# Kernel tuning notes

Hardware: AMD Instinct MI355X
Metric: run time of the kernel (lower is better)

The kernel has to match this reference:

```python
import jax, jax.numpy as jnp
import numpy as np

B, K, L, D = 64, 64, 128, 128  # batch, top_k, max_length, embedding_dimension
H = 2 * D                      # MLP input size (context || gathered entity)
N_HIDDEN = 6                   # Linear(H,H) layers with Tanh (dropout is eval no-op)


def setup_inputs() -> dict:
    key = jax.random.key(0)
    k0, k1, k2 = jax.random.split(key, 3)
    context = jax.random.normal(k0, (B, K, 2, L, D), dtype=jnp.float32)
    Ws = jax.random.normal(k1, (N_HIDDEN, H, H), dtype=jnp.float32) * 0.05
    bs = jnp.zeros((N_HIDDEN, H), dtype=jnp.float32)
    W_out = jax.random.normal(k2, (H,), dtype=jnp.float32) * 0.05
    b_out = jnp.zeros((), dtype=jnp.float32)
    return {"context": context, "Ws": Ws, "bs": bs, "W_out": W_out, "b_out": b_out}


def reference(context, Ws, bs, W_out, b_out):
    ctx = context[:, :, 0]  # [B,K,L,D]
    ent = context[:, :, 1]  # [B,K,L,D]
    cn = jnp.linalg.norm(ctx, axis=-1, keepdims=True)  # [B,K,L,1]
    en = jnp.linalg.norm(ent, axis=-1, keepdims=True)  # [B,K,L,1]
    # cosine-similarity matrix between context rows and entity rows
    sim = jnp.einsum("bkld,bkmd->bklm", ctx, ent) / (cn * jnp.swapaxes(en, -1, -2))
    ctx_n = ctx / cn
    ent_n = ent / en
    idx = jnp.argmax(sim, axis=-1)  # [B,K,L] top-1 entity row per context row
    gathered = jnp.take_along_axis(
        ent_n, jnp.broadcast_to(idx[..., None], ent_n.shape), axis=2
    )  # [B,K,L,D]
    # stack(...,-2) then flatten(start_dim=-2) == concat along feature dim
    x = jnp.concatenate([ctx_n, gathered], axis=-1)  # [B,K,L,2D]
    for i in range(N_HIDDEN):
        x = jnp.tanh(x @ Ws[i].T + bs[i])
    out = x @ W_out + b_out  # [B,K,L]
    return jnp.sum(out, axis=-1)  # [B,K] (sum over L then squeeze)
```

## Files before the change

kernel.cpp:

```cpp
#include <hip/hip_runtime.h>

#define FID4(r,c4) ((r)*128 + ((((c4) ^ ((r)&31))) << 2))
#define FIDS(r,c)  ((r)*128 + (((((c)>>2) ^ ((r)&31))) << 2) + ((c)&3))
#define XIDX(r,c)  ((r)*256 + (((((c)>>3) ^ ((r)&7))) << 3) + ((c)&7))

typedef _Float16 half_t;
typedef __attribute__((ext_vector_type(8))) _Float16 f16x8;
typedef __attribute__((ext_vector_type(4))) float f32x4;

__device__ __forceinline__ float tanh_fast(float x){
    float e = __expf(2.0f * x);
    return 1.0f - 2.0f / (e + 1.0f);
}

__device__ __forceinline__ f16x8 cvt8(float4 a, float4 b){
    f16x8 r;
    r[0]=(half_t)a.x; r[1]=(half_t)a.y; r[2]=(half_t)a.z; r[3]=(half_t)a.w;
    r[4]=(half_t)b.x; r[5]=(half_t)b.y; r[6]=(half_t)b.z; r[7]=(half_t)b.w;
    return r;
}

__global__ __launch_bounds__(512)
__attribute__((amdgpu_waves_per_eu(2, 2)))
void fused_mlp_som(const float* __restrict__ ctx_in,
                   const float* __restrict__ Ws,
                   const float* __restrict__ bs,
                   const float* __restrict__ Wout,
                   const float* __restrict__ bout,
                   float* __restrict__ out)
{
    extern __shared__ char smem[];
    float* ctxS   = (float*)smem;
    float* entS   = ctxS + 128*128;
    float* inv_cn = entS + 128*128;
    float* inv_en = inv_cn + 128;
    int*   idxm   = (int*)(inv_en + 128);
    float* redbuf = (float*)(idxm + 128);
    half_t* xf = (half_t*)smem;

    const int tid  = threadIdx.x;
    const int lane = tid & 63;
    const int bk   = blockIdx.x;

    const float4* gbase = (const float4*)(ctx_in + (size_t)bk * (2*128*128));
    #pragma unroll
    for (int it = 0; it < 8; ++it){
        int fi = tid + 512*it;
        int r  = fi >> 5;
        int c4 = fi & 31;
        float4 v = gbase[fi];
        *(float4*)&ctxS[FID4(r,c4)] = v;
        float4 e = gbase[fi + 4096];
        *(float4*)&entS[FID4(r,c4)] = e;
    }
    __syncthreads();

    {
        int hf = tid & 1;
        int r  = (tid >> 1) & 127;
        const float* tile = (tid < 256) ? ctxS : entS;
        float s = 0.f;
        #pragma unroll
        for (int u = 0; u < 16; ++u){
            float4 v = *(const float4*)&tile[FID4(r, 16*hf + u)];
            s = fmaf(v.x, v.x, s); s = fmaf(v.y, v.y, s);
            s = fmaf(v.z, v.z, s); s = fmaf(v.w, v.w, s);
        }
        s += __shfl_xor(s, 1);
        if (hf == 0){
            float inv = 1.0f / sqrtf(s);
            if (tid < 256) inv_cn[r] = inv; else inv_en[r] = inv;
        }
    }
    __syncthreads();

    {
        const int ti = tid >> 5;
        const int tj = tid & 31;
        const int l0 = ti * 8;
        float acc[8][4];
        #pragma unroll
        for (int i = 0; i < 8; ++i)
            #pragma unroll
            for (int j = 0; j < 4; ++j) acc[i][j] = 0.f;

        for (int kc = 0; kc < 32; ++kc){
            float4 e0 = *(const float4*)&entS[FID4(tj     , kc)];
            float4 e1 = *(const float4*)&entS[FID4(tj + 32, kc)];
            float4 e2 = *(const float4*)&entS[FID4(tj + 64, kc)];
            float4 e3 = *(const float4*)&entS[FID4(tj + 96, kc)];
            #pragma unroll
            for (int i = 0; i < 8; ++i){
                float4 a = *(const float4*)&ctxS[FID4(l0+i, kc)];
                acc[i][0] = fmaf(a.x,e0.x,acc[i][0]); acc[i][0] = fmaf(a.y,e0.y,acc[i][0]);
                acc[i][0] = fmaf(a.z,e0.z,acc[i][0]); acc[i][0] = fmaf(a.w,e0.w,acc[i][0]);
                acc[i][1] = fmaf(a.x,e1.x,acc[i][1]); acc[i][1] = fmaf(a.y,e1.y,acc[i][1]);
                acc[i][1] = fmaf(a.z,e1.z,acc[i][1]); acc[i][1] = fmaf(a.w,e1.w,acc[i][1]);
                acc[i][2] = fmaf(a.x,e2.x,acc[i][2]); acc[i][2] = fmaf(a.y,e2.y,acc[i][2]);
                acc[i][2] = fmaf(a.z,e2.z,acc[i][2]); acc[i][2] = fmaf(a.w,e2.w,acc[i][2]);
                acc[i][3] = fmaf(a.x,e3.x,acc[i][3]); acc[i][3] = fmaf(a.y,e3.y,acc[i][3]);
                acc[i][3] = fmaf(a.z,e3.z,acc[i][3]); acc[i][3] = fmaf(a.w,e3.w,acc[i][3]);
            }
        }
        #pragma unroll
        for (int i = 0; i < 8; ++i){
            float best = -1e38f; int bi = 0;
            #pragma unroll
            for (int j = 0; j < 4; ++j){
                int m = tj + 32*j;
                float v = acc[i][j] * inv_en[m];
                if (v > best || (v == best && m < bi)){ best = v; bi = m; }
            }
            #pragma unroll
            for (int s = 1; s < 32; s <<= 1){
                float ov = __shfl_xor(best, s);
                int   oi = __shfl_xor(bi,   s);
                if (ov > best || (ov == best && oi < bi)){ best = ov; bi = oi; }
            }
            if (tj == 0) idxm[l0 + i] = bi;
        }
    }
    __syncthreads();

    {
        const int c  = tid & 255;
        const int hb = tid >> 8;
        half_t pk[64];
        #pragma unroll
        for (int r = 0; r < 64; ++r){
            int l = hb*64 + r;
            float v;
            if (c < 128){
                v = ctxS[FIDS(l, c)] * inv_cn[l];
            } else {
                int mi = idxm[l];
                v = entS[FIDS(mi, c-128)] * inv_en[mi];
            }
            pk[r] = (half_t)v;
        }
        __syncthreads();
        #pragma unroll
        for (int r = 0; r < 64; ++r){
            int l = hb*64 + r;
            xf[XIDX(l, c)] = pk[r];
        }
    }
    __syncthreads();

    const int wv    = tid >> 6;
    const int lan15 = lane & 15;
    const int lq    = lane >> 4;
    const int n0    = 32*wv + lan15;
    const int n1    = n0 + 16;
    const int bno0  = n0 * 256;
    const int bno1  = n1 * 256;
    const int kb    = 8*lq;

    float4 p0a = *(const float4*)&Ws[bno0 + kb];
    float4 p0b = *(const float4*)&Ws[bno0 + kb + 4];
    float4 p1a = *(const float4*)&Ws[bno1 + kb];
    float4 p1b = *(const float4*)&Ws[bno1 + kb + 4];

    #pragma unroll 1
    for (int layer = 0; layer < 6; ++layer){
        const float* WsL = Ws + layer*65536;
        const float* WsN = Ws + ((layer < 5) ? (layer+1) : 5)*65536;

        f32x4 acc[8][2];
        #pragma unroll
        for (int mt = 0; mt < 8; ++mt){
            acc[mt][0] = (f32x4){0.f,0.f,0.f,0.f};
            acc[mt][1] = (f32x4){0.f,0.f,0.f,0.f};
        }

        #pragma unroll 1
        for (int ks = 0; ks < 8; ++ks){
            const int aoff = (((4*ks + lq) ^ (lan15 & 7)) << 3);
            f16x8 a[8];
            #pragma unroll
            for (int mt = 0; mt < 8; ++mt)
                a[mt] = *(const f16x8*)&xf[(16*mt + lan15)*256 + aoff];
            f16x8 b0 = cvt8(p0a, p0b);
            f16x8 b1 = cvt8(p1a, p1b);
            const float* pW = (ks < 7) ? WsL : WsN;
            const int kn = (ks < 7) ? (32*(ks+1) + kb) : kb;
            p0a = *(const float4*)&pW[bno0 + kn];
            p0b = *(const float4*)&pW[bno0 + kn + 4];
            p1a = *(const float4*)&pW[bno1 + kn];
            p1b = *(const float4*)&pW[bno1 + kn + 4];
            #pragma unroll
            for (int mt = 0; mt < 8; ++mt){
                acc[mt][0] = __builtin_amdgcn_mfma_f32_16x16x32_f16(a[mt], b0, acc[mt][0], 0,0,0);
                acc[mt][1] = __builtin_amdgcn_mfma_f32_16x16x32_f16(a[mt], b1, acc[mt][1], 0,0,0);
            }
        }
        __syncthreads();

        if (layer < 5){
            float bias0 = bs[layer*256 + n0];
            float bias1 = bs[layer*256 + n1];
            #pragma unroll
            for (int mt = 0; mt < 8; ++mt){
                #pragma unroll
                for (int r = 0; r < 4; ++r){
                    int row = 16*mt + 4*lq + r;
                    xf[XIDX(row, n0)] = (half_t)tanh_fast(acc[mt][0][r] + bias0);
                    xf[XIDX(row, n1)] = (half_t)tanh_fast(acc[mt][1][r] + bias1);
                }
            }
            __syncthreads();
        } else {
            float bias0 = bs[5*256 + n0];
            float bias1 = bs[5*256 + n1];
            float w0 = Wout[n0];
            float w1 = Wout[n1];
            float part = 0.f;
            #pragma unroll
            for (int mt = 0; mt < 8; ++mt){
                #pragma unroll
                for (int r = 0; r < 4; ++r){
                    part = fmaf(tanh_fast(acc[mt][0][r] + bias0), w0, part);
                    part = fmaf(tanh_fast(acc[mt][1][r] + bias1), w1, part);
                }
            }
            #pragma unroll
            for (int s = 1; s < 64; s <<= 1) part += __shfl_xor(part, s);
            if (lane == 0) redbuf[wv] = part;
            __syncthreads();
            if (tid == 0){
                float s = 0.f;
                #pragma unroll
                for (int i = 0; i < 8; ++i) s += redbuf[i];
                out[bk] = s + 128.0f * bout[0];
            }
        }
    }
}

extern "C" void kernel_launch(void* const* d_in, const int* in_sizes, int n_in,
                              void* d_out, int out_size, void* d_ws, size_t ws_size,
                              hipStream_t stream)
{
    (void)in_sizes; (void)n_in; (void)out_size; (void)d_ws; (void)ws_size;
    const float* ctx  = (const float*)d_in[0];
    const float* Ws   = (const float*)d_in[1];
    const float* bs   = (const float*)d_in[2];
    const float* Wout = (const float*)d_in[3];
    const float* bout = (const float*)d_in[4];
    float* out = (float*)d_out;

    const int smem_bytes = 2*128*128*4 + 128*4 + 128*4 + 128*4 + 8*4;
    hipFuncSetAttribute(reinterpret_cast<const void*>(fused_mlp_som),
                        hipFuncAttributeMaxDynamicSharedMemorySize, smem_bytes);
    fused_mlp_som<<<dim3(4096), dim3(512), smem_bytes, stream>>>(ctx, Ws, bs, Wout, bout, out);
}
```

Before: 1.616 ms.

## Halve block size, drop entity LDS tile, widen per-wave MFMA tiles

Blocks shrink from 512 to 256 threads and the entity tile is no longer staged in shared memory. Entity rows are read directly from global memory for the norms, the similarity loop (with a one-step register prefetch) and the gather. Halving LDS per block (64KB) is meant to allow two blocks per CU. Each wave now computes 64 output columns with 4 MFMA N-fragments, so each A fragment is reused more. The costs are higher register pressure from the 16x4 and 8x4 accumulators, and uncoalesced, L2-dependent global reads of entity rows.

Result: slower. 2.059 ms (+27.4%).

```diff
diff --git a/kernel.cpp b/kernel.cpp
--- a/kernel.cpp
+++ b/kernel.cpp
@@ -20,8 +20,7 @@
     return r;
 }
 
-__global__ __launch_bounds__(512)
-__attribute__((amdgpu_waves_per_eu(2, 2)))
+__global__ __launch_bounds__(256, 2)
 void fused_mlp_som(const float* __restrict__ ctx_in,
                    const float* __restrict__ Ws,
                    const float* __restrict__ bs,
@@ -31,8 +30,7 @@
 {
     extern __shared__ char smem[];
     float* ctxS   = (float*)smem;
-    float* entS   = ctxS + 128*128;
-    float* inv_cn = entS + 128*128;
+    float* inv_cn = ctxS + 128*128;
     float* inv_en = inv_cn + 128;
     int*   idxm   = (int*)(inv_en + 128);
     float* redbuf = (float*)(idxm + 128);
@@ -42,34 +40,42 @@
     const int lane = tid & 63;
     const int bk   = blockIdx.x;
 
-    const float4* gbase = (const float4*)(ctx_in + (size_t)bk * (2*128*128));
-    #pragma unroll
-    for (int it = 0; it < 8; ++it){
-        int fi = tid + 512*it;
-        int r  = fi >> 5;
-        int c4 = fi & 31;
-        float4 v = gbase[fi];
-        *(float4*)&ctxS[FID4(r,c4)] = v;
-        float4 e = gbase[fi + 4096];
-        *(float4*)&entS[FID4(r,c4)] = e;
+    const float* gctx = ctx_in + (size_t)bk * 32768;
+    const float* gent = gctx + 16384;
+
+    {
+        const float4* gb = (const float4*)gctx;
+        #pragma unroll
+        for (int it = 0; it < 16; ++it){
+            int fi = tid + 256*it;
+            int r  = fi >> 5;
+            int c4 = fi & 31;
+            *(float4*)&ctxS[FID4(r,c4)] = gb[fi];
+        }
     }
     __syncthreads();
 
     {
         int hf = tid & 1;
-        int r  = (tid >> 1) & 127;
-        const float* tile = (tid < 256) ? ctxS : entS;
-        float s = 0.f;
+        int r  = tid >> 1;
+        float s = 0.f, t = 0.f;
         #pragma unroll
         for (int u = 0; u < 16; ++u){
-            float4 v = *(const float4*)&tile[FID4(r, 16*hf + u)];
+            float4 v = *(const float4*)&ctxS[FID4(r, 16*hf + u)];
             s = fmaf(v.x, v.x, s); s = fmaf(v.y, v.y, s);
             s = fmaf(v.z, v.z, s); s = fmaf(v.w, v.w, s);
         }
+        #pragma unroll
+        for (int u = 0; u < 16; ++u){
+            float4 v = *(const float4*)&gent[r*128 + 64*hf + 4*u];
+            t = fmaf(v.x, v.x, t); t = fmaf(v.y, v.y, t);
+            t = fmaf(v.z, v.z, t); t = fmaf(v.w, v.w, t);
+        }
         s += __shfl_xor(s, 1);
+        t += __shfl_xor(t, 1);
         if (hf == 0){
-            float inv = 1.0f / sqrtf(s);
-            if (tid < 256) inv_cn[r] = inv; else inv_en[r] = inv;
+            inv_cn[r] = 1.0f / sqrtf(s);
+            inv_en[r] = 1.0f / sqrtf(t);
         }
     }
     __syncthreads();
@@ -77,20 +83,25 @@
     {
         const int ti = tid >> 5;
         const int tj = tid & 31;
-        const int l0 = ti * 8;
-        float acc[8][4];
-        #pragma unroll
-        for (int i = 0; i < 8; ++i)
+        const int l0 = ti * 16;
+        float acc[16][4];
+        #pragma unroll
+        for (int i = 0; i < 16; ++i)
             #pragma unroll
             for (int j = 0; j < 4; ++j) acc[i][j] = 0.f;
 
+        float4 e0 = *(const float4*)&gent[(tj      )*128];
+        float4 e1 = *(const float4*)&gent[(tj + 32 )*128];
+        float4 e2 = *(const float4*)&gent[(tj + 64 )*128];
+        float4 e3 = *(const float4*)&gent[(tj + 96 )*128];
         for (int kc = 0; kc < 32; ++kc){
-            float4 e0 = *(const float4*)&entS[FID4(tj     , kc)];
-            float4 e1 = *(const float4*)&entS[FID4(tj + 32, kc)];
-            float4 e2 = *(const float4*)&entS[FID4(tj + 64, kc)];
-            float4 e3 = *(const float4*)&entS[FID4(tj + 96, kc)];
-            #pragma unroll
-            for (int i = 0; i < 8; ++i){
+            const int kn = ((kc+1)&31) << 2;
+            float4 f0 = *(const float4*)&gent[(tj      )*128 + kn];
+            float4 f1 = *(const float4*)&gent[(tj + 32 )*128 + kn];
+            float4 f2 = *(const float4*)&gent[(tj + 64 )*128 + kn];
+            float4 f3 = *(const float4*)&gent[(tj + 96 )*128 + kn];
+            #pragma unroll
+            for (int i = 0; i < 16; ++i){
                 float4 a = *(const float4*)&ctxS[FID4(l0+i, kc)];
                 acc[i][0] = fmaf(a.x,e0.x,acc[i][0]); acc[i][0] = fmaf(a.y,e0.y,acc[i][0]);
                 acc[i][0] = fmaf(a.z,e0.z,acc[i][0]); acc[i][0] = fmaf(a.w,e0.w,acc[i][0]);
@@ -101,9 +112,10 @@
                 acc[i][3] = fmaf(a.x,e3.x,acc[i][3]); acc[i][3] = fmaf(a.y,e3.y,acc[i][3]);
                 acc[i][3] = fmaf(a.z,e3.z,acc[i][3]); acc[i][3] = fmaf(a.w,e3.w,acc[i][3]);
             }
-        }
-        #pragma unroll
-        for (int i = 0; i < 8; ++i){
+            e0=f0; e1=f1; e2=f2; e3=f3;
+        }
+        #pragma unroll
+        for (int i = 0; i < 16; ++i){
             float best = -1e38f; int bi = 0;
             #pragma unroll
             for (int j = 0; j < 4; ++j){
@@ -123,55 +135,57 @@
     __syncthreads();
 
     {
-        const int c  = tid & 255;
-        const int hb = tid >> 8;
-        half_t pk[64];
-        #pragma unroll
-        for (int r = 0; r < 64; ++r){
-            int l = hb*64 + r;
-            float v;
-            if (c < 128){
-                v = ctxS[FIDS(l, c)] * inv_cn[l];
-            } else {
-                int mi = idxm[l];
-                v = entS[FIDS(mi, c-128)] * inv_en[mi];
-            }
-            pk[r] = (half_t)v;
-        }
-        __syncthreads();
-        #pragma unroll
-        for (int r = 0; r < 64; ++r){
-            int l = hb*64 + r;
-            xf[XIDX(l, c)] = pk[r];
-        }
-    }
-    __syncthreads();
+        const int c = tid;
+        #pragma unroll 1
+        for (int hb = 0; hb < 2; ++hb){
+            half_t pk[64];
+            #pragma unroll
+            for (int r = 0; r < 64; ++r){
+                int l = hb*64 + r;
+                float v;
+                if (c < 128){
+                    v = ctxS[FIDS(l, c)] * inv_cn[l];
+                } else {
+                    int mi = idxm[l];
+                    v = gent[mi*128 + (c-128)] * inv_en[mi];
+                }
+                pk[r] = (half_t)v;
+            }
+            __syncthreads();
+            #pragma unroll
+            for (int r = 0; r < 64; ++r){
+                int l = hb*64 + r;
+                xf[XIDX(l, c)] = pk[r];
+            }
+            __syncthreads();
+        }
+    }
 
     const int wv    = tid >> 6;
     const int lan15 = lane & 15;
     const int lq    = lane >> 4;
-    const int n0    = 32*wv + lan15;
-    const int n1    = n0 + 16;
-    const int bno0  = n0 * 256;
-    const int bno1  = n1 * 256;
     const int kb    = 8*lq;
-
-    float4 p0a = *(const float4*)&Ws[bno0 + kb];
-    float4 p0b = *(const float4*)&Ws[bno0 + kb + 4];
-    float4 p1a = *(const float4*)&Ws[bno1 + kb];
-    float4 p1b = *(const float4*)&Ws[bno1 + kb + 4];
+    const int aBase = lan15*256;
+
+    float4 pA[4], pB[4];
+    #pragma unroll
+    for (int nf = 0; nf < 4; ++nf){
+        int bn = (64*wv + 16*nf + lan15)*256;
+        pA[nf] = *(const float4*)&Ws[bn + kb];
+        pB[nf] = *(const float4*)&Ws[bn + kb + 4];
+    }
 
     #pragma unroll 1
     for (int layer = 0; layer < 6; ++layer){
         const float* WsL = Ws + layer*65536;
         const float* WsN = Ws + ((layer < 5) ? (layer+1) : 5)*65536;
 
-        f32x4 acc[8][2];
-        #pragma unroll
-        for (int mt = 0; mt < 8; ++mt){
-            acc[mt][0] = (f32x4){0.f,0.f,0.f,0.f};
-            acc[mt][1] = (f32x4){0.f,0.f,0.f,0.f};
-        }
+        f32x4 acc[8][4];
+        #pragma unroll
+        for (int mt = 0; mt < 8; ++mt)
+            #pragma unroll
+            for (int nf = 0; nf < 4; ++nf)
+                acc[mt][nf] = (f32x4){0.f,0.f,0.f,0.f};
 
         #pragma unroll 1
         for (int ks = 0; ks < 8; ++ks){
@@ -179,58 +193,65 @@
             f16x8 a[8];
             #pragma unroll
             for (int mt = 0; mt < 8; ++mt)
-                a[mt] = *(const f16x8*)&xf[(16*mt + lan15)*256 + aoff];
-            f16x8 b0 = cvt8(p0a, p0b);
-            f16x8 b1 = cvt8(p1a, p1b);
+                a[mt] = *(const f16x8*)&xf[aBase + mt*4096 + aoff];
+            f16x8 b[4];
+            #pragma unroll
+            for (int nf = 0; nf < 4; ++nf) b[nf] = cvt8(pA[nf], pB[nf]);
             const float* pW = (ks < 7) ? WsL : WsN;
             const int kn = (ks < 7) ? (32*(ks+1) + kb) : kb;
-            p0a = *(const float4*)&pW[bno0 + kn];
-            p0b = *(const float4*)&pW[bno0 + kn + 4];
-            p1a = *(const float4*)&pW[bno1 + kn];
-            p1b = *(const float4*)&pW[bno1 + kn + 4];
-            #pragma unroll
-            for (int mt = 0; mt < 8; ++mt){
-                acc[mt][0] = __builtin_amdgcn_mfma_f32_16x16x32_f16(a[mt], b0, acc[mt][0], 0,0,0);
-                acc[mt][1] = __builtin_amdgcn_mfma_f32_16x16x32_f16(a[mt], b1, acc[mt][1], 0,0,0);
-            }
+            #pragma unroll
+            for (int nf = 0; nf < 4; ++nf){
+                int bn = (64*wv + 16*nf + lan15)*256;
+                pA[nf] = *(const float4*)&pW[bn + kn];
+                pB[nf] = *(const float4*)&pW[bn + kn + 4];
+            }
+            #pragma unroll
+            for (int mt = 0; mt < 8; ++mt)
+                #pragma unroll
+                for (int nf = 0; nf < 4; ++nf)
+                    acc[mt][nf] = __builtin_amdgcn_mfma_f32_16x16x32_f16(a[mt], b[nf], acc[mt][nf], 0,0,0);
         }
         __syncthreads();
 
         if (layer < 5){
-            float bias0 = bs[layer*256 + n0];
-            float bias1 = bs[layer*256 + n1];
+            float bias[4];
+            #pragma unroll
+            for (int nf = 0; nf < 4; ++nf) bias[nf] = bs[layer*256 + 64*wv + 16*nf + lan15];
             #pragma unroll
             for (int mt = 0; mt < 8; ++mt){
                 #pragma unroll
-                for (int r = 0; r < 4; ++r){
-                    int row = 16*mt + 4*lq + r;
-                    xf[XIDX(row, n0)] = (half_t)tanh_fast(acc[mt][0][r] + bias0);
-                    xf[XIDX(row, n1)] = (half_t)tanh_fast(acc[mt][1][r] + bias1);
+                for (int nf = 0; nf < 4; ++nf){
+                    const int n = 64*wv + 16*nf + lan15;
+                    #pragma unroll
+                    for (int r = 0; r < 4; ++r){
+                        int row = 16*mt + 4*lq + r;
+                        xf[XIDX(row, n)] = (half_t)tanh_fast(acc[mt][nf][r] + bias[nf]);
+                    }
                 }
             }
             __syncthreads();
         } else {
-            float bias0 = bs[5*256 + n0];
-            float bias1 = bs[5*256 + n1];
-            float w0 = Wout[n0];
-            float w1 = Wout[n1];
+            float bias[4], w[4];
+            #pragma unroll
+            for (int nf = 0; nf < 4; ++nf){
+                const int n = 64*wv + 16*nf + lan15;
+                bias[nf] = bs[5*256 + n];
+                w[nf]    = Wout[n];
+            }
             float part = 0.f;
             #pragma unroll
-            for (int mt = 0; mt < 8; ++mt){
+            for (int mt = 0; mt < 8; ++mt)
                 #pragma unroll
-                for (int r = 0; r < 4; ++r){
-                    part = fmaf(tanh_fast(acc[mt][0][r] + bias0), w0, part);
-                    part = fmaf(tanh_fast(acc[mt][1][r] + bias1), w1, part);
-                }
-            }
+                for (int nf = 0; nf < 4; ++nf)
+                    #pragma unroll
+                    for (int r = 0; r < 4; ++r)
+                        part = fmaf(tanh_fast(acc[mt][nf][r] + bias[nf]), w[nf], part);
             #pragma unroll
             for (int s = 1; s < 64; s <<= 1) part += __shfl_xor(part, s);
             if (lane == 0) redbuf[wv] = part;
             __syncthreads();
             if (tid == 0){
-                float s = 0.f;
-                #pragma unroll
-                for (int i = 0; i < 8; ++i) s += redbuf[i];
+                float s = redbuf[0] + redbuf[1] + redbuf[2] + redbuf[3];
                 out[bk] = s + 128.0f * bout[0];
             }
         }
@@ -249,8 +270,8 @@
     const float* bout = (const float*)d_in[4];
     float* out = (float*)d_out;
 
-    const int smem_bytes = 2*128*128*4 + 128*4 + 128*4 + 128*4 + 8*4;
+    const int smem_bytes = 128*128*4 + 128*4 + 128*4 + 128*4 + 4*4;
     hipFuncSetAttribute(reinterpret_cast<const void*>(fused_mlp_som),
                         hipFuncAttributeMaxDynamicSharedMemorySize, smem_bytes);
-    fused_mlp_som<<<dim3(4096), dim3(512), smem_bytes, stream>>>(ctx, Ws, bs, Wout, bout, out);
-}
+    fused_mlp_som<<<dim3(4096), dim3(256), smem_bytes, stream>>>(ctx, Ws, bs, Wout, bout, out);
+}
```
